# Kernel optimization log

Measured on AMD Instinct MI355X. Metric: run time of the kernel, lower is better.

Reference implementation:

```python
import jax, jax.numpy as jnp
import numpy as np

B, S, D, H = 2, 2048, 1024, 16
DK = D // H


def setup_inputs() -> dict:
    key = jax.random.key(0)
    ks = jax.random.split(key, 10)
    scale = 1.0 / np.sqrt(D)
    x = jax.random.normal(ks[0], (B, S, D), dtype=jnp.float32)
    # causal mask: 1 = attend, 0 = masked (module's create_causal_mask)
    mask = jnp.tril(jnp.ones((S, S), dtype=jnp.int32))[None, None]
    Wq = jax.random.normal(ks[1], (D, D), jnp.float32) * scale
    bq = jax.random.normal(ks[2], (D,), jnp.float32) * 0.01
    Wk = jax.random.normal(ks[3], (D, D), jnp.float32) * scale
    bk = jax.random.normal(ks[4], (D,), jnp.float32) * 0.01
    Wv = jax.random.normal(ks[5], (D, D), jnp.float32) * scale
    bv = jax.random.normal(ks[6], (D,), jnp.float32) * 0.01
    Wo = jax.random.normal(ks[7], (D, D), jnp.float32) * scale
    bo = jax.random.normal(ks[8], (D,), jnp.float32) * 0.01
    return {"x": x, "mask": mask, "Wq": Wq, "bq": bq, "Wk": Wk, "bk": bk,
            "Wv": Wv, "bv": bv, "Wo": Wo, "bo": bo}


def reference(x, mask, Wq, bq, Wk, bk, Wv, bv, Wo, bo):
    b, s, _ = x.shape
    # projections; [B,S,D] -> [B,H,S,DK]
    def split_heads(t):
        return t.reshape(b, s, H, DK).transpose(0, 2, 1, 3)
    Q = split_heads(x @ Wq + bq)
    K = split_heads(x @ Wk + bk)
    V = split_heads(x @ Wv + bv)
    scores = jnp.einsum('bhqd,bhkd->bhqk', Q, K) / np.sqrt(DK)
    scores = jnp.where(mask == 0, jnp.float32(-1e9), scores)
    attn = jax.nn.softmax(scores, axis=-1)  # dropout p=0 -> identity
    ctx = jnp.einsum('bhqk,bhkd->bhqd', attn, V)
    ctx = ctx.transpose(0, 2, 1, 3).reshape(b, s, D)
    return ctx @ Wo + bo
```

## Files before the change

### kernel.cpp

```cpp
#include <hip/hip_runtime.h>
#include <hip/hip_bf16.h>


typedef _Float16 f16x8 __attribute__((ext_vector_type(8)));
typedef _Float16 f16x4 __attribute__((ext_vector_type(4)));
typedef _Float16 f16x2 __attribute__((ext_vector_type(2)));
typedef float f32x4 __attribute__((ext_vector_type(4)));

#define QSCALE 0.180336880111112f

__device__ __forceinline__ void async_copy16(const _Float16* gsrc,
                                             _Float16* ldst) {
  __builtin_amdgcn_global_load_lds(
      (const __attribute__((address_space(1))) void*)gsrc,
      (__attribute__((address_space(3))) void*)ldst, 16, 0, 0);
}

__global__ __launch_bounds__(256) void prep(
    const float* __restrict__ x, _Float16* __restrict__ xh,
    const float* __restrict__ W0, const float* __restrict__ W1,
    const float* __restrict__ W2, const float* __restrict__ W3,
    _Float16* __restrict__ T0, _Float16* __restrict__ T1,
    _Float16* __restrict__ T2, _Float16* __restrict__ T3) {
  if (blockIdx.x < 4096) {
    int i = (blockIdx.x * 256 + threadIdx.x) * 4;
    float4 v = *(const float4*)(x + i);
    f16x4 o;
    o.x = (_Float16)v.x; o.y = (_Float16)v.y;
    o.z = (_Float16)v.z; o.w = (_Float16)v.w;
    *(f16x4*)(xh + i) = o;
    return;
  }
  const int id = blockIdx.x - 4096;
  const int w = id >> 10, rem = id & 1023;
  const int bx = rem & 31, by = rem >> 5;
  const float* W; _Float16* T;
  switch (w) {
    case 0: W = W0; T = T0; break;
    case 1: W = W1; T = T1; break;
    case 2: W = W2; T = T2; break;
    default: W = W3; T = T3; break;
  }
  __shared__ _Float16 tile[32][33];
  const int tx = threadIdx.x & 31, ty = threadIdx.x >> 5;
  const int n0 = bx * 32, k0 = by * 32;
  for (int i = 0; i < 4; i++) {
    int kk = k0 + ty + i * 8;
    tile[ty + i * 8][tx] = (_Float16)W[(size_t)kk * 1024 + n0 + tx];
  }
  __syncthreads();
  for (int i = 0; i < 4; i++) {
    int nn = n0 + ty + i * 8;
    T[(size_t)nn * 1024 + k0 + tx] = tile[tx][ty + i * 8];
  }
}

__global__ __launch_bounds__(256) void gemm_qkv(
    const _Float16* __restrict__ A, const _Float16* __restrict__ BtAll,
    const float* __restrict__ bq, const float* __restrict__ bk,
    const float* __restrict__ bv, _Float16* __restrict__ Qh,
    _Float16* __restrict__ Kh, _Float16* __restrict__ VT) {
  __shared__ _Float16 As[128 * 32];
  __shared__ _Float16 Bs[128 * 32];
  __shared__ _Float16 tbuf[64 * 136];
  const int tid = threadIdx.x;
  const int wave = tid >> 6, lane = tid & 63;
  const int lr = lane & 15, lq = lane >> 4;
  const int m0 = blockIdx.x * 128, n0 = blockIdx.y * 128;
  const int rw = (wave & 1) * 64, cw = (wave >> 1) * 64;

  const int sel = blockIdx.y >> 3;
  const float* bias = sel == 0 ? bq : (sel == 1 ? bk : bv);
  const int c0 = n0 & 1023;

  f32x4 acc[4][4] = {};
  const int r0 = wave * 32 + (lane >> 2);
  const int woff = (lane & 3) * 8;

  for (int kt = 0; kt < 1024; kt += 32) {
    __syncthreads();
    async_copy16(A + (size_t)(m0 + r0) * 1024 + kt + woff, As + r0 * 32 + woff);
    async_copy16(A + (size_t)(m0 + r0 + 16) * 1024 + kt + woff,
                 As + (r0 + 16) * 32 + woff);
    async_copy16(BtAll + (size_t)(n0 + r0) * 1024 + kt + woff,
                 Bs + r0 * 32 + woff);
    async_copy16(BtAll + (size_t)(n0 + r0 + 16) * 1024 + kt + woff,
                 Bs + (r0 + 16) * 32 + woff);
    __syncthreads();
    f16x8 af[4], bf[4];
    for (int i = 0; i < 4; i++)
      af[i] = *(const f16x8*)(As + (rw + i * 16 + lr) * 32 + lq * 8);
    for (int j = 0; j < 4; j++)
      bf[j] = *(const f16x8*)(Bs + (cw + j * 16 + lr) * 32 + lq * 8);
    for (int i = 0; i < 4; i++)
      for (int j = 0; j < 4; j++)
        acc[i][j] = __builtin_amdgcn_mfma_f32_16x16x32_f16(af[i], bf[j],
                                                           acc[i][j], 0, 0, 0);
  }

  if (sel == 2) {
    const int bb = m0 >> 11, ss0 = m0 & 2047;
    const int cs = tid & 15, dkr = tid >> 4;
    for (int jj = 0; jj < 2; jj++) {
      __syncthreads();
      if ((wave >> 1) == jj) {
        for (int i = 0; i < 4; i++) {
          const int sl = rw + i * 16 + lq * 4;
          for (int j = 0; j < 4; j++) {
            const int dk = j * 16 + lr;
            const float bvl = bias[c0 + jj * 64 + dk];
            f16x4 pv;
            for (int r = 0; r < 4; r++) pv[r] = (_Float16)(acc[i][j][r] + bvl);
            *(f16x4*)(tbuf + dk * 136 + sl) = pv;
          }
        }
      }
      __syncthreads();
      const int hh = (c0 + jj * 64) >> 6;
      _Float16* dst = VT + ((size_t)(bb * 16 + hh) * 64) * 2048 + ss0;
      for (int k = 0; k < 4; k++) {
        const int dk = dkr + k * 16;
        *(uint4*)(dst + (size_t)dk * 2048 + cs * 8) =
            *(const uint4*)(tbuf + dk * 136 + cs * 8);
      }
    }
  } else {
    _Float16* out = sel == 0 ? Qh : Kh;
    const float scl = sel == 0 ? QSCALE : 1.0f;
    for (int i = 0; i < 4; i++) {
      const int row = m0 + rw + i * 16 + lq * 4;
      for (int j = 0; j < 4; j++) {
        const int col = c0 + cw + j * 16 + lr;
        const float bvl = bias[col];
        for (int r = 0; r < 4; r++)
          out[(size_t)(row + r) * 1024 + col] =
              (_Float16)((acc[i][j][r] + bvl) * scl);
      }
    }
  }
}

__global__ __launch_bounds__(256) void gemm_out(
    const _Float16* __restrict__ A, const _Float16* __restrict__ Bt,
    const float* __restrict__ bias, float* __restrict__ out) {
  __shared__ _Float16 As[128 * 32];
  __shared__ _Float16 Bs[64 * 32];
  const int tid = threadIdx.x;
  const int wave = tid >> 6, lane = tid & 63;
  const int lr = lane & 15, lq = lane >> 4;
  const int m0 = blockIdx.x * 128, n0 = blockIdx.y * 64;
  const int rw = (wave & 1) * 64, cw = (wave >> 1) * 32;
  f32x4 acc[4][2] = {};
  const int r0 = wave * 32 + (lane >> 2);
  const int br = tid >> 2;
  const int woff = (lane & 3) * 8;

  for (int kt = 0; kt < 1024; kt += 32) {
    __syncthreads();
    async_copy16(A + (size_t)(m0 + r0) * 1024 + kt + woff, As + r0 * 32 + woff);
    async_copy16(A + (size_t)(m0 + r0 + 16) * 1024 + kt + woff,
                 As + (r0 + 16) * 32 + woff);
    async_copy16(Bt + (size_t)(n0 + br) * 1024 + kt + woff,
                 Bs + br * 32 + woff);
    __syncthreads();
    f16x8 af[4], bf[2];
    for (int i = 0; i < 4; i++)
      af[i] = *(const f16x8*)(As + (rw + i * 16 + lr) * 32 + lq * 8);
    for (int j = 0; j < 2; j++)
      bf[j] = *(const f16x8*)(Bs + (cw + j * 16 + lr) * 32 + lq * 8);
    for (int i = 0; i < 4; i++)
      for (int j = 0; j < 2; j++)
        acc[i][j] = __builtin_amdgcn_mfma_f32_16x16x32_f16(af[i], bf[j],
                                                           acc[i][j], 0, 0, 0);
  }
  for (int i = 0; i < 4; i++) {
    const int row = m0 + rw + i * 16 + lq * 4;
    for (int j = 0; j < 2; j++) {
      const int col = n0 + cw + j * 16 + lr;
      const float bvl = bias[col];
      for (int r = 0; r < 4; r++)
        out[(size_t)(row + r) * 1024 + col] = acc[i][j][r] + bvl;
    }
  }
}

__global__ __launch_bounds__(512, 4) void attn(const _Float16* __restrict__ Q,
                                               const _Float16* __restrict__ K,
                                               const _Float16* __restrict__ VT,
                                               _Float16* __restrict__ ctx) {
  const int sp = blockIdx.y;
  const int bh = blockIdx.x;
  const int b = bh >> 4, h = bh & 15;
  const int tid = threadIdx.x, wave = tid >> 6, lane = tid & 63;
  const int lr = lane & 15, lq = lane >> 4;
  const int rg = wave & 1;
  const int kvq = wave >> 1;
  const int kho = kvq * 16;
  const size_t qkbase = ((size_t)b * 2048) * 1024 + h * 64;
  const size_t vtbase = ((size_t)bh) * 64 * 2048;

  __shared__ __align__(16) char smem[45056];

  f16x4 onesf;
  {
    _Float16 ov = (lr == 0) ? (_Float16)1.0f : (_Float16)0.0f;
    for (int i = 0; i < 4; i++) onesf[i] = ov;
  }

  const int sgr = tid >> 3, sc8 = tid & 7;
  const int ssw = sgr * 64 + ((sc8 ^ (sgr & 7)) * 8);
  const _Float16* Kg0 = K + qkbase + (size_t)sgr * 1024 + sc8 * 8;
  const _Float16* Vg0 = VT + vtbase + (size_t)sgr * 2048 + sc8 * 8;

  for (int ph = 0; ph < 2; ph++) {
    const int st = ph ? 31 - sp : sp;
    const int qmin = st * 64 + rg * 32;
    const _Float16* qp = Q + qkbase + (size_t)(qmin + lr) * 1024 + lq * 8;
    f16x8 qA0 = *(const f16x8*)qp;
    f16x8 qA1 = *(const f16x8*)(qp + 32);
    f16x8 qB0 = *(const f16x8*)(qp + (size_t)16 * 1024);
    f16x8 qB1 = *(const f16x8*)(qp + (size_t)16 * 1024 + 32);

    f32x4 oA[4] = {}, oB[4] = {};
    f32x4 olA = {}, olB = {};

    uint4 ka = *(const uint4*)Kg0;
    uint4 va = *(const uint4*)Vg0;

    for (int t = 0; t <= st; t++) {
      _Float16* ksb = (_Float16*)(smem + (t & 1) * 8192);
      _Float16* vsb = (_Float16*)(smem + 16384 + (t & 1) * 8192);
      *(uint4*)(ksb + ssw) = ka;
      *(uint4*)(vsb + ssw) = va;
      __syncthreads();
      if (t < st) {
        const _Float16* kg = Kg0 + (size_t)(t + 1) * 64 * 1024;
        const _Float16* vg = Vg0 + (t + 1) * 64;
        ka = *(const uint4*)kg;
        va = *(const uint4*)vg;
      }
      const int kvw = t * 64 + kho;
      if (kvw > qmin + 31) continue;

      const int krow = kho + lr;
      const int ksw = krow & 7;
      f16x8 k0 = *(const f16x8*)(ksb + krow * 64 + ((lq ^ ksw) * 8));
      f16x8 k1 = *(const f16x8*)(ksb + krow * 64 + (((lq + 4) ^ ksw) * 8));

      f32x4 sA = {}, sB = {};
      sA = __builtin_amdgcn_mfma_f32_16x16x32_f16(k0, qA0, sA, 0, 0, 0);
      sA = __builtin_amdgcn_mfma_f32_16x16x32_f16(k1, qA1, sA, 0, 0, 0);
      sB = __builtin_amdgcn_mfma_f32_16x16x32_f16(k0, qB0, sB, 0, 0, 0);
      sB = __builtin_amdgcn_mfma_f32_16x16x32_f16(k1, qB1, sB, 0, 0, 0);

      if (kvw + 15 > qmin) {
        const int qcol = qmin + lr;
        for (int r = 0; r < 4; r++)
          if (kvw + lq * 4 + r > qcol) sA[r] = -1e30f;
      }
      if (kvw + 15 > qmin + 16) {
        const int qcol = qmin + 16 + lr;
        for (int r = 0; r < 4; r++)
          if (kvw + lq * 4 + r > qcol) sB[r] = -1e30f;
      }

      f16x4 paA, paB;
      {
        float p0 = exp2f(sA[0]), p1 = exp2f(sA[1]);
        float p2 = exp2f(sA[2]), p3 = exp2f(sA[3]);
        f16x2 q01 =
            __builtin_bit_cast(f16x2, __builtin_amdgcn_cvt_pkrtz(p0, p1));
        f16x2 q23 =
            __builtin_bit_cast(f16x2, __builtin_amdgcn_cvt_pkrtz(p2, p3));
        paA = __builtin_shufflevector(q01, q23, 0, 1, 2, 3);
      }
      {
        float p0 = exp2f(sB[0]), p1 = exp2f(sB[1]);
        float p2 = exp2f(sB[2]), p3 = exp2f(sB[3]);
        f16x2 q01 =
            __builtin_bit_cast(f16x2, __builtin_amdgcn_cvt_pkrtz(p0, p1));
        f16x2 q23 =
            __builtin_bit_cast(f16x2, __builtin_amdgcn_cvt_pkrtz(p2, p3));
        paB = __builtin_shufflevector(q01, q23, 0, 1, 2, 3);
      }

      __builtin_amdgcn_s_setprio(1);
      const int vc8 = kvq * 2 + (lq >> 1), vsub = (lq & 1) * 4;
      for (int dn = 0; dn < 4; dn++) {
        const int vrow = dn * 16 + lr;
        f16x4 vf = *(const f16x4*)(vsb + vrow * 64 +
                                   ((vc8 ^ (vrow & 7)) * 8) + vsub);
        oA[dn] = __builtin_amdgcn_mfma_f32_16x16x16f16(paA, vf, oA[dn], 0, 0, 0);
        oB[dn] = __builtin_amdgcn_mfma_f32_16x16x16f16(paB, vf, oB[dn], 0, 0, 0);
      }
      olA = __builtin_amdgcn_mfma_f32_16x16x16f16(paA, onesf, olA, 0, 0, 0);
      olB = __builtin_amdgcn_mfma_f32_16x16x16f16(paB, onesf, olB, 0, 0, 0);
      __builtin_amdgcn_s_setprio(0);
    }

    float* const cb = (float*)smem;
    __syncthreads();
    if (kvq == 1 || kvq == 3) {
      float* p = cb + (((kvq == 1 ? 0 : 2) + rg) * 64 + lane) * 44;
      *(f32x4*)(p + 0) = oA[0];  *(f32x4*)(p + 4) = oA[1];
      *(f32x4*)(p + 8) = oA[2];  *(f32x4*)(p + 12) = oA[3];
      *(f32x4*)(p + 16) = oB[0]; *(f32x4*)(p + 20) = oB[1];
      *(f32x4*)(p + 24) = oB[2]; *(f32x4*)(p + 28) = oB[3];
      *(f32x4*)(p + 32) = olA;   *(f32x4*)(p + 36) = olB;
    }
    __syncthreads();
    if (kvq == 0 || kvq == 2) {
      float* p = cb + (((kvq == 0 ? 0 : 2) + rg) * 64 + lane) * 44;
      oA[0] += *(const f32x4*)(p + 0);  oA[1] += *(const f32x4*)(p + 4);
      oA[2] += *(const f32x4*)(p + 8);  oA[3] += *(const f32x4*)(p + 12);
      oB[0] += *(const f32x4*)(p + 16); oB[1] += *(const f32x4*)(p + 20);
      oB[2] += *(const f32x4*)(p + 24); oB[3] += *(const f32x4*)(p + 28);
      olA += *(const f32x4*)(p + 32);   olB += *(const f32x4*)(p + 36);
      if (kvq == 2) {
        *(f32x4*)(p + 0) = oA[0];  *(f32x4*)(p + 4) = oA[1];
        *(f32x4*)(p + 8) = oA[2];  *(f32x4*)(p + 12) = oA[3];
        *(f32x4*)(p + 16) = oB[0]; *(f32x4*)(p + 20) = oB[1];
        *(f32x4*)(p + 24) = oB[2]; *(f32x4*)(p + 28) = oB[3];
        *(f32x4*)(p + 32) = olA;   *(f32x4*)(p + 36) = olB;
      }
    }
    __syncthreads();
    if (kvq == 0) {
      const float* p = cb + ((2 + rg) * 64 + lane) * 44;
      oA[0] += *(const f32x4*)(p + 0);  oA[1] += *(const f32x4*)(p + 4);
      oA[2] += *(const f32x4*)(p + 8);  oA[3] += *(const f32x4*)(p + 12);
      oB[0] += *(const f32x4*)(p + 16); oB[1] += *(const f32x4*)(p + 20);
      oB[2] += *(const f32x4*)(p + 24); oB[3] += *(const f32x4*)(p + 28);
      olA += *(const f32x4*)(p + 32);   olB += *(const f32x4*)(p + 36);
      for (int r = 0; r < 4; r++) {
        float lvA = __shfl(olA[r], lane & 48);
        float invA = 1.0f / lvA;
        const int rowA = qmin + lq * 4 + r;
        for (int dn = 0; dn < 4; dn++)
          ctx[qkbase + (size_t)rowA * 1024 + dn * 16 + lr] =
              (_Float16)(oA[dn][r] * invA);
        float lvB = __shfl(olB[r], lane & 48);
        float invB = 1.0f / lvB;
        const int rowB = qmin + 16 + lq * 4 + r;
        for (int dn = 0; dn < 4; dn++)
          ctx[qkbase + (size_t)rowB * 1024 + dn * 16 + lr] =
              (_Float16)(oB[dn][r] * invB);
      }
    }
    __syncthreads();
  }
}

extern "C" void kernel_launch(void* const* d_in, const int* in_sizes, int n_in,
                              void* d_out, int out_size, void* d_ws,
                              size_t ws_size, hipStream_t stream) {
  const float* x  = (const float*)d_in[0];
  const float* Wq = (const float*)d_in[2];
  const float* bq = (const float*)d_in[3];
  const float* Wk = (const float*)d_in[4];
  const float* bk = (const float*)d_in[5];
  const float* Wv = (const float*)d_in[6];
  const float* bv = (const float*)d_in[7];
  const float* Wo = (const float*)d_in[8];
  const float* bo = (const float*)d_in[9];
  float* out = (float*)d_out;

  char* ws = (char*)d_ws;
  const size_t MB = 1 << 20;
  _Float16* xh  = (_Float16*)(ws);
  _Float16* WTs = (_Float16*)(ws + 8 * MB);
  _Float16* WqT = WTs;
  _Float16* WkT = (_Float16*)(ws + 10 * MB);
  _Float16* WvT = (_Float16*)(ws + 12 * MB);
  _Float16* WoT = (_Float16*)(ws + 14 * MB);
  _Float16* Qh  = (_Float16*)(ws + 16 * MB);
  _Float16* Kh  = (_Float16*)(ws + 24 * MB);
  _Float16* VT  = (_Float16*)(ws + 32 * MB);
  _Float16* ctx = (_Float16*)(ws);

  prep<<<8192, 256, 0, stream>>>(x, xh, Wq, Wk, Wv, Wo, WqT, WkT, WvT, WoT);
  gemm_qkv<<<dim3(32, 24), 256, 0, stream>>>(xh, WTs, bq, bk, bv, Qh, Kh, VT);
  attn<<<dim3(32, 16), 512, 0, stream>>>(Qh, Kh, VT, ctx);
  gemm_out<<<dim3(32, 16), 256, 0, stream>>>(ctx, WoT, bo, out);
}
```

Measured before the change: 191.0 us.

## Enlarge attention KV tile to 128 keys per barrier step

Each loop iteration now stages 128 keys of K and V^T into double-buffered shared memory instead of 64, and each wave handles two 16-key slices inside an unrolled inner loop. This halves the number of __syncthreads barriers and global-to-LDS staging rounds per query tile, which cuts synchronisation overhead. In exchange shared memory rises from 44 KB to 64 KB per block, which may reduce occupancy under the 4-blocks launch bound, and the causal edge wastes more work on partially masked tiles.

```diff
diff --git a/kernel.cpp b/kernel.cpp
--- a/kernel.cpp
+++ b/kernel.cpp
@@ -195,11 +195,10 @@
   const int lr = lane & 15, lq = lane >> 4;
   const int rg = wave & 1;
   const int kvq = wave >> 1;
-  const int kho = kvq * 16;
   const size_t qkbase = ((size_t)b * 2048) * 1024 + h * 64;
   const size_t vtbase = ((size_t)bh) * 64 * 2048;
 
-  __shared__ __align__(16) char smem[45056];
+  __shared__ __align__(16) char smem[65536];
 
   f16x4 onesf;
   {
@@ -207,10 +206,14 @@
     for (int i = 0; i < 4; i++) onesf[i] = ov;
   }
 
-  const int sgr = tid >> 3, sc8 = tid & 7;
-  const int ssw = sgr * 64 + ((sc8 ^ (sgr & 7)) * 8);
-  const _Float16* Kg0 = K + qkbase + (size_t)sgr * 1024 + sc8 * 8;
-  const _Float16* Vg0 = VT + vtbase + (size_t)sgr * 2048 + sc8 * 8;
+  const int kr = tid >> 2, kc = tid & 3;
+  const int kw0 = kr * 64 + ((kc ^ (kr & 7)) * 8);
+  const int kw1 = kr * 64 + (((kc + 4) ^ (kr & 7)) * 8);
+  const _Float16* Kg0 = K + qkbase + (size_t)kr * 1024 + kc * 8;
+  const int vr = tid >> 3, vc = tid & 7;
+  const int vw0 = vr * 128 + ((vc ^ (vr & 7)) * 8);
+  const int vw1 = vr * 128 + (((vc + 8) ^ (vr & 7)) * 8);
+  const _Float16* Vg0 = VT + vtbase + (size_t)vr * 2048 + vc * 8;
 
   for (int ph = 0; ph < 2; ph++) {
     const int st = ph ? 31 - sp : sp;
@@ -224,78 +227,89 @@
     f32x4 oA[4] = {}, oB[4] = {};
     f32x4 olA = {}, olB = {};
 
-    uint4 ka = *(const uint4*)Kg0;
-    uint4 va = *(const uint4*)Vg0;
-
-    for (int t = 0; t <= st; t++) {
-      _Float16* ksb = (_Float16*)(smem + (t & 1) * 8192);
-      _Float16* vsb = (_Float16*)(smem + 16384 + (t & 1) * 8192);
-      *(uint4*)(ksb + ssw) = ka;
-      *(uint4*)(vsb + ssw) = va;
+    const int tmax = (st * 64 + 63) >> 7;
+
+    uint4 ka0 = *(const uint4*)Kg0, ka1 = *(const uint4*)(Kg0 + 32);
+    uint4 va0 = *(const uint4*)Vg0, va1 = *(const uint4*)(Vg0 + 64);
+
+    for (int t = 0; t <= tmax; t++) {
+      _Float16* ksb = (_Float16*)(smem + (t & 1) * 16384);
+      _Float16* vsb = (_Float16*)(smem + 32768 + (t & 1) * 16384);
+      *(uint4*)(ksb + kw0) = ka0;
+      *(uint4*)(ksb + kw1) = ka1;
+      *(uint4*)(vsb + vw0) = va0;
+      *(uint4*)(vsb + vw1) = va1;
       __syncthreads();
-      if (t < st) {
-        const _Float16* kg = Kg0 + (size_t)(t + 1) * 64 * 1024;
-        const _Float16* vg = Vg0 + (t + 1) * 64;
-        ka = *(const uint4*)kg;
-        va = *(const uint4*)vg;
-      }
-      const int kvw = t * 64 + kho;
-      if (kvw > qmin + 31) continue;
-
-      const int krow = kho + lr;
-      const int ksw = krow & 7;
-      f16x8 k0 = *(const f16x8*)(ksb + krow * 64 + ((lq ^ ksw) * 8));
-      f16x8 k1 = *(const f16x8*)(ksb + krow * 64 + (((lq + 4) ^ ksw) * 8));
-
-      f32x4 sA = {}, sB = {};
-      sA = __builtin_amdgcn_mfma_f32_16x16x32_f16(k0, qA0, sA, 0, 0, 0);
-      sA = __builtin_amdgcn_mfma_f32_16x16x32_f16(k1, qA1, sA, 0, 0, 0);
-      sB = __builtin_amdgcn_mfma_f32_16x16x32_f16(k0, qB0, sB, 0, 0, 0);
-      sB = __builtin_amdgcn_mfma_f32_16x16x32_f16(k1, qB1, sB, 0, 0, 0);
-
-      if (kvw + 15 > qmin) {
-        const int qcol = qmin + lr;
-        for (int r = 0; r < 4; r++)
-          if (kvw + lq * 4 + r > qcol) sA[r] = -1e30f;
-      }
-      if (kvw + 15 > qmin + 16) {
-        const int qcol = qmin + 16 + lr;
-        for (int r = 0; r < 4; r++)
-          if (kvw + lq * 4 + r > qcol) sB[r] = -1e30f;
-      }
-
-      f16x4 paA, paB;
-      {
-        float p0 = exp2f(sA[0]), p1 = exp2f(sA[1]);
-        float p2 = exp2f(sA[2]), p3 = exp2f(sA[3]);
-        f16x2 q01 =
-            __builtin_bit_cast(f16x2, __builtin_amdgcn_cvt_pkrtz(p0, p1));
-        f16x2 q23 =
-            __builtin_bit_cast(f16x2, __builtin_amdgcn_cvt_pkrtz(p2, p3));
-        paA = __builtin_shufflevector(q01, q23, 0, 1, 2, 3);
-      }
-      {
-        float p0 = exp2f(sB[0]), p1 = exp2f(sB[1]);
-        float p2 = exp2f(sB[2]), p3 = exp2f(sB[3]);
-        f16x2 q01 =
-            __builtin_bit_cast(f16x2, __builtin_amdgcn_cvt_pkrtz(p0, p1));
-        f16x2 q23 =
-            __builtin_bit_cast(f16x2, __builtin_amdgcn_cvt_pkrtz(p2, p3));
-        paB = __builtin_shufflevector(q01, q23, 0, 1, 2, 3);
-      }
-
-      __builtin_amdgcn_s_setprio(1);
-      const int vc8 = kvq * 2 + (lq >> 1), vsub = (lq & 1) * 4;
-      for (int dn = 0; dn < 4; dn++) {
-        const int vrow = dn * 16 + lr;
-        f16x4 vf = *(const f16x4*)(vsb + vrow * 64 +
-                                   ((vc8 ^ (vrow & 7)) * 8) + vsub);
-        oA[dn] = __builtin_amdgcn_mfma_f32_16x16x16f16(paA, vf, oA[dn], 0, 0, 0);
-        oB[dn] = __builtin_amdgcn_mfma_f32_16x16x16f16(paB, vf, oB[dn], 0, 0, 0);
-      }
-      olA = __builtin_amdgcn_mfma_f32_16x16x16f16(paA, onesf, olA, 0, 0, 0);
-      olB = __builtin_amdgcn_mfma_f32_16x16x16f16(paB, onesf, olB, 0, 0, 0);
-      __builtin_amdgcn_s_setprio(0);
+      if (t < tmax) {
+        const _Float16* kg = Kg0 + (size_t)(t + 1) * 131072;
+        const _Float16* vg = Vg0 + (t + 1) * 128;
+        ka0 = *(const uint4*)kg; ka1 = *(const uint4*)(kg + 32);
+        va0 = *(const uint4*)vg; va1 = *(const uint4*)(vg + 64);
+      }
+      if (t * 128 + kvq * 32 > qmin + 31) continue;
+
+#pragma unroll
+      for (int ksl = 0; ksl < 2; ksl++) {
+        const int kvw = t * 128 + kvq * 32 + ksl * 16;
+        if (kvw > qmin + 31) break;
+
+        const int krow = kvq * 32 + ksl * 16 + lr;
+        const int ksw = krow & 7;
+        f16x8 k0 = *(const f16x8*)(ksb + krow * 64 + ((lq ^ ksw) * 8));
+        f16x8 k1 = *(const f16x8*)(ksb + krow * 64 + (((lq + 4) ^ ksw) * 8));
+
+        f32x4 sA = {}, sB = {};
+        sA = __builtin_amdgcn_mfma_f32_16x16x32_f16(k0, qA0, sA, 0, 0, 0);
+        sA = __builtin_amdgcn_mfma_f32_16x16x32_f16(k1, qA1, sA, 0, 0, 0);
+        sB = __builtin_amdgcn_mfma_f32_16x16x32_f16(k0, qB0, sB, 0, 0, 0);
+        sB = __builtin_amdgcn_mfma_f32_16x16x32_f16(k1, qB1, sB, 0, 0, 0);
+
+        if (kvw + 15 > qmin) {
+          const int qcol = qmin + lr;
+          for (int r = 0; r < 4; r++)
+            if (kvw + lq * 4 + r > qcol) sA[r] = -1e30f;
+        }
+        if (kvw + 15 > qmin + 16) {
+          const int qcol = qmin + 16 + lr;
+          for (int r = 0; r < 4; r++)
+            if (kvw + lq * 4 + r > qcol) sB[r] = -1e30f;
+        }
+
+        f16x4 paA, paB;
+        {
+          float p0 = exp2f(sA[0]), p1 = exp2f(sA[1]);
+          float p2 = exp2f(sA[2]), p3 = exp2f(sA[3]);
+          f16x2 q01 =
+              __builtin_bit_cast(f16x2, __builtin_amdgcn_cvt_pkrtz(p0, p1));
+          f16x2 q23 =
+              __builtin_bit_cast(f16x2, __builtin_amdgcn_cvt_pkrtz(p2, p3));
+          paA = __builtin_shufflevector(q01, q23, 0, 1, 2, 3);
+        }
+        {
+          float p0 = exp2f(sB[0]), p1 = exp2f(sB[1]);
+          float p2 = exp2f(sB[2]), p3 = exp2f(sB[3]);
+          f16x2 q01 =
+              __builtin_bit_cast(f16x2, __builtin_amdgcn_cvt_pkrtz(p0, p1));
+          f16x2 q23 =
+              __builtin_bit_cast(f16x2, __builtin_amdgcn_cvt_pkrtz(p2, p3));
+          paB = __builtin_shufflevector(q01, q23, 0, 1, 2, 3);
+        }
+
+        __builtin_amdgcn_s_setprio(1);
+        const int vc8 = kvq * 4 + ksl * 2 + (lq >> 1), vsub = (lq & 1) * 4;
+        for (int dn = 0; dn < 4; dn++) {
+          const int vrow = dn * 16 + lr;
+          f16x4 vf = *(const f16x4*)(vsb + vrow * 128 +
+                                     ((vc8 ^ (vrow & 7)) * 8) + vsub);
+          oA[dn] =
+              __builtin_amdgcn_mfma_f32_16x16x16f16(paA, vf, oA[dn], 0, 0, 0);
+          oB[dn] =
+              __builtin_amdgcn_mfma_f32_16x16x16f16(paB, vf, oB[dn], 0, 0, 0);
+        }
+        olA = __builtin_amdgcn_mfma_f32_16x16x16f16(paA, onesf, olA, 0, 0, 0);
+        olB = __builtin_amdgcn_mfma_f32_16x16x16f16(paB, onesf, olB, 0, 0, 0);
+        __builtin_amdgcn_s_setprio(0);
+      }
     }
 
     float* const cb = (float*)smem;
```

New measurement: 196.1 us. +2.7%, slower.

## Split attention blocks into 32-row query tiles with 4 waves per block

Applied to the files above, without the earlier changes.

The attention kernel now uses 256-thread blocks that each handle one 32-row query tile, instead of 512-thread blocks covering two 32-row groups of a 64-row tile. The grid doubles to 32x32, and causal pairing now runs over 64 tiles (j and 63-j). Each thread stages two 16-byte chunks of K and V per step, and shared memory drops to 32 KB. The aim is finer-grained load balance and higher occupancy. The cost is that K/V tiles are reloaded from global memory twice as often across blocks.

```diff
diff --git a/kernel.cpp b/kernel.cpp
--- a/kernel.cpp
+++ b/kernel.cpp
@@ -184,7 +184,7 @@
   }
 }
 
-__global__ __launch_bounds__(512, 4) void attn(const _Float16* __restrict__ Q,
+__global__ __launch_bounds__(256, 4) void attn(const _Float16* __restrict__ Q,
                                                const _Float16* __restrict__ K,
                                                const _Float16* __restrict__ VT,
                                                _Float16* __restrict__ ctx) {
@@ -193,13 +193,12 @@
   const int b = bh >> 4, h = bh & 15;
   const int tid = threadIdx.x, wave = tid >> 6, lane = tid & 63;
   const int lr = lane & 15, lq = lane >> 4;
-  const int rg = wave & 1;
-  const int kvq = wave >> 1;
+  const int kvq = wave;
   const int kho = kvq * 16;
   const size_t qkbase = ((size_t)b * 2048) * 1024 + h * 64;
   const size_t vtbase = ((size_t)bh) * 64 * 2048;
 
-  __shared__ __align__(16) char smem[45056];
+  __shared__ __align__(16) char smem[32768];
 
   f16x4 onesf;
   {
@@ -207,14 +206,15 @@
     for (int i = 0; i < 4; i++) onesf[i] = ov;
   }
 
-  const int sgr = tid >> 3, sc8 = tid & 7;
-  const int ssw = sgr * 64 + ((sc8 ^ (sgr & 7)) * 8);
-  const _Float16* Kg0 = K + qkbase + (size_t)sgr * 1024 + sc8 * 8;
-  const _Float16* Vg0 = VT + vtbase + (size_t)sgr * 2048 + sc8 * 8;
+  const int sgr = tid >> 2, sc = tid & 3;
+  const int sw0 = sgr * 64 + ((sc ^ (sgr & 7)) * 8);
+  const int sw1 = sgr * 64 + (((sc + 4) ^ (sgr & 7)) * 8);
+  const _Float16* Kg0 = K + qkbase + (size_t)sgr * 1024 + sc * 8;
+  const _Float16* Vg0 = VT + vtbase + (size_t)sgr * 2048 + sc * 8;
 
   for (int ph = 0; ph < 2; ph++) {
-    const int st = ph ? 31 - sp : sp;
-    const int qmin = st * 64 + rg * 32;
+    const int j = ph ? 63 - sp : sp;
+    const int qmin = j * 32;
     const _Float16* qp = Q + qkbase + (size_t)(qmin + lr) * 1024 + lq * 8;
     f16x8 qA0 = *(const f16x8*)qp;
     f16x8 qA1 = *(const f16x8*)(qp + 32);
@@ -224,20 +224,24 @@
     f32x4 oA[4] = {}, oB[4] = {};
     f32x4 olA = {}, olB = {};
 
-    uint4 ka = *(const uint4*)Kg0;
-    uint4 va = *(const uint4*)Vg0;
-
-    for (int t = 0; t <= st; t++) {
+    const int tmax = (qmin + 31) >> 6;
+
+    uint4 ka = *(const uint4*)Kg0, kb = *(const uint4*)(Kg0 + 32);
+    uint4 va = *(const uint4*)Vg0, vb = *(const uint4*)(Vg0 + 32);
+
+    for (int t = 0; t <= tmax; t++) {
       _Float16* ksb = (_Float16*)(smem + (t & 1) * 8192);
       _Float16* vsb = (_Float16*)(smem + 16384 + (t & 1) * 8192);
-      *(uint4*)(ksb + ssw) = ka;
-      *(uint4*)(vsb + ssw) = va;
+      *(uint4*)(ksb + sw0) = ka;
+      *(uint4*)(ksb + sw1) = kb;
+      *(uint4*)(vsb + sw0) = va;
+      *(uint4*)(vsb + sw1) = vb;
       __syncthreads();
-      if (t < st) {
-        const _Float16* kg = Kg0 + (size_t)(t + 1) * 64 * 1024;
+      if (t < tmax) {
+        const _Float16* kg = Kg0 + (size_t)(t + 1) * 65536;
         const _Float16* vg = Vg0 + (t + 1) * 64;
-        ka = *(const uint4*)kg;
-        va = *(const uint4*)vg;
+        ka = *(const uint4*)kg; kb = *(const uint4*)(kg + 32);
+        va = *(const uint4*)vg; vb = *(const uint4*)(vg + 32);
       }
       const int kvw = t * 64 + kho;
       if (kvw > qmin + 31) continue;
@@ -300,8 +304,8 @@
 
     float* const cb = (float*)smem;
     __syncthreads();
-    if (kvq == 1 || kvq == 3) {
-      float* p = cb + (((kvq == 1 ? 0 : 2) + rg) * 64 + lane) * 44;
+    if (wave & 1) {
+      float* p = cb + ((wave >> 1) * 64 + lane) * 44;
       *(f32x4*)(p + 0) = oA[0];  *(f32x4*)(p + 4) = oA[1];
       *(f32x4*)(p + 8) = oA[2];  *(f32x4*)(p + 12) = oA[3];
       *(f32x4*)(p + 16) = oB[0]; *(f32x4*)(p + 20) = oB[1];
@@ -309,14 +313,14 @@
       *(f32x4*)(p + 32) = olA;   *(f32x4*)(p + 36) = olB;
     }
     __syncthreads();
-    if (kvq == 0 || kvq == 2) {
-      float* p = cb + (((kvq == 0 ? 0 : 2) + rg) * 64 + lane) * 44;
+    if (!(wave & 1)) {
+      float* p = cb + ((wave >> 1) * 64 + lane) * 44;
       oA[0] += *(const f32x4*)(p + 0);  oA[1] += *(const f32x4*)(p + 4);
       oA[2] += *(const f32x4*)(p + 8);  oA[3] += *(const f32x4*)(p + 12);
       oB[0] += *(const f32x4*)(p + 16); oB[1] += *(const f32x4*)(p + 20);
       oB[2] += *(const f32x4*)(p + 24); oB[3] += *(const f32x4*)(p + 28);
       olA += *(const f32x4*)(p + 32);   olB += *(const f32x4*)(p + 36);
-      if (kvq == 2) {
+      if (wave == 2) {
         *(f32x4*)(p + 0) = oA[0];  *(f32x4*)(p + 4) = oA[1];
         *(f32x4*)(p + 8) = oA[2];  *(f32x4*)(p + 12) = oA[3];
         *(f32x4*)(p + 16) = oB[0]; *(f32x4*)(p + 20) = oB[1];
@@ -325,8 +329,8 @@
       }
     }
     __syncthreads();
-    if (kvq == 0) {
-      const float* p = cb + ((2 + rg) * 64 + lane) * 44;
+    if (wave == 0) {
+      const float* p = cb + (64 + lane) * 44;
       oA[0] += *(const f32x4*)(p + 0);  oA[1] += *(const f32x4*)(p + 4);
       oA[2] += *(const f32x4*)(p + 8);  oA[3] += *(const f32x4*)(p + 12);
       oB[0] += *(const f32x4*)(p + 16); oB[1] += *(const f32x4*)(p + 20);
@@ -380,6 +384,6 @@
 
   prep<<<8192, 256, 0, stream>>>(x, xh, Wq, Wk, Wv, Wo, WqT, WkT, WvT, WoT);
   gemm_qkv<<<dim3(32, 24), 256, 0, stream>>>(xh, WTs, bq, bk, bv, Qh, Kh, VT);
-  attn<<<dim3(32, 16), 512, 0, stream>>>(Qh, Kh, VT, ctx);
+  attn<<<dim3(32, 32), 256, 0, stream>>>(Qh, Kh, VT, ctx);
   gemm_out<<<dim3(32, 16), 256, 0, stream>>>(ctx, WoT, bo, out);
 }
```

New measurement: 197.6 us. 3.5% more time.

## Double GEMM K-tile to 64 with XOR-swizzled LDS layout

Applied to the files above, without the earlier changes.

Both the QKV and output-projection GEMMs now stage 64-wide K tiles instead of 32, halving the number of barrier pairs per K loop. Global columns are XOR-swizzled by row on load so the fragment reads from LDS avoid bank conflicts with the wider 128-byte rows. The QKV kernel also aliases its transpose buffer onto the same shared memory, keeping LDS use at 32KB. The trade-off is a larger LDS footprint per block, which may reduce occupancy, and the loop is still single-buffered with no prefetch.

```diff
diff --git a/kernel.cpp b/kernel.cpp
--- a/kernel.cpp
+++ b/kernel.cpp
@@ -60,9 +60,9 @@
     const float* __restrict__ bq, const float* __restrict__ bk,
     const float* __restrict__ bv, _Float16* __restrict__ Qh,
     _Float16* __restrict__ Kh, _Float16* __restrict__ VT) {
-  __shared__ _Float16 As[128 * 32];
-  __shared__ _Float16 Bs[128 * 32];
-  __shared__ _Float16 tbuf[64 * 136];
+  __shared__ __align__(16) char smem[32768];
+  _Float16* As = (_Float16*)smem;
+  _Float16* Bs = (_Float16*)(smem + 16384);
   const int tid = threadIdx.x;
   const int wave = tid >> 6, lane = tid & 63;
   const int lr = lane & 15, lq = lane >> 4;
@@ -74,31 +74,42 @@
   const int c0 = n0 & 1023;
 
   f32x4 acc[4][4] = {};
-  const int r0 = wave * 32 + (lane >> 2);
-  const int woff = (lane & 3) * 8;
-
-  for (int kt = 0; kt < 1024; kt += 32) {
-    __syncthreads();
-    async_copy16(A + (size_t)(m0 + r0) * 1024 + kt + woff, As + r0 * 32 + woff);
-    async_copy16(A + (size_t)(m0 + r0 + 16) * 1024 + kt + woff,
-                 As + (r0 + 16) * 32 + woff);
-    async_copy16(BtAll + (size_t)(n0 + r0) * 1024 + kt + woff,
-                 Bs + r0 * 32 + woff);
-    async_copy16(BtAll + (size_t)(n0 + r0 + 16) * 1024 + kt + woff,
-                 Bs + (r0 + 16) * 32 + woff);
-    __syncthreads();
-    f16x8 af[4], bf[4];
-    for (int i = 0; i < 4; i++)
-      af[i] = *(const f16x8*)(As + (rw + i * 16 + lr) * 32 + lq * 8);
-    for (int j = 0; j < 4; j++)
-      bf[j] = *(const f16x8*)(Bs + (cw + j * 16 + lr) * 32 + lq * 8);
-    for (int i = 0; i < 4; i++)
-      for (int j = 0; j < 4; j++)
-        acc[i][j] = __builtin_amdgcn_mfma_f32_16x16x32_f16(af[i], bf[j],
-                                                           acc[i][j], 0, 0, 0);
+  const int sr = lane >> 3;
+  const int srow = wave * 32 + sr;
+  const int sgc = (((lane & 7) ^ sr)) * 8;
+  const int sldst = srow * 64 + (lane & 7) * 8;
+  const int lrx = lr & 7;
+
+  for (int kt = 0; kt < 1024; kt += 64) {
+    __syncthreads();
+#pragma unroll
+    for (int off = 0; off < 32; off += 8) {
+      async_copy16(A + (size_t)(m0 + srow + off) * 1024 + kt + sgc,
+                   As + sldst + off * 64);
+      async_copy16(BtAll + (size_t)(n0 + srow + off) * 1024 + kt + sgc,
+                   Bs + sldst + off * 64);
+    }
+    __syncthreads();
+#pragma unroll
+    for (int kk = 0; kk < 2; kk++) {
+      f16x8 af[4], bf[4];
+      for (int i = 0; i < 4; i++) {
+        const int ar = rw + i * 16 + lr;
+        af[i] = *(const f16x8*)(As + ar * 64 + (((kk * 4 + lq) ^ lrx) * 8));
+      }
+      for (int j = 0; j < 4; j++) {
+        const int br = cw + j * 16 + lr;
+        bf[j] = *(const f16x8*)(Bs + br * 64 + (((kk * 4 + lq) ^ lrx) * 8));
+      }
+      for (int i = 0; i < 4; i++)
+        for (int j = 0; j < 4; j++)
+          acc[i][j] = __builtin_amdgcn_mfma_f32_16x16x32_f16(
+              af[i], bf[j], acc[i][j], 0, 0, 0);
+    }
   }
 
   if (sel == 2) {
+    _Float16* tbuf = (_Float16*)smem;
     const int bb = m0 >> 11, ss0 = m0 & 2047;
     const int cs = tid & 15, dkr = tid >> 4;
     for (int jj = 0; jj < 2; jj++) {
@@ -143,35 +154,50 @@
 __global__ __launch_bounds__(256) void gemm_out(
     const _Float16* __restrict__ A, const _Float16* __restrict__ Bt,
     const float* __restrict__ bias, float* __restrict__ out) {
-  __shared__ _Float16 As[128 * 32];
-  __shared__ _Float16 Bs[64 * 32];
+  __shared__ __align__(16) char smem[24576];
+  _Float16* As = (_Float16*)smem;
+  _Float16* Bs = (_Float16*)(smem + 16384);
   const int tid = threadIdx.x;
   const int wave = tid >> 6, lane = tid & 63;
   const int lr = lane & 15, lq = lane >> 4;
   const int m0 = blockIdx.x * 128, n0 = blockIdx.y * 64;
   const int rw = (wave & 1) * 64, cw = (wave >> 1) * 32;
   f32x4 acc[4][2] = {};
-  const int r0 = wave * 32 + (lane >> 2);
-  const int br = tid >> 2;
-  const int woff = (lane & 3) * 8;
-
-  for (int kt = 0; kt < 1024; kt += 32) {
-    __syncthreads();
-    async_copy16(A + (size_t)(m0 + r0) * 1024 + kt + woff, As + r0 * 32 + woff);
-    async_copy16(A + (size_t)(m0 + r0 + 16) * 1024 + kt + woff,
-                 As + (r0 + 16) * 32 + woff);
-    async_copy16(Bt + (size_t)(n0 + br) * 1024 + kt + woff,
-                 Bs + br * 32 + woff);
-    __syncthreads();
-    f16x8 af[4], bf[2];
-    for (int i = 0; i < 4; i++)
-      af[i] = *(const f16x8*)(As + (rw + i * 16 + lr) * 32 + lq * 8);
-    for (int j = 0; j < 2; j++)
-      bf[j] = *(const f16x8*)(Bs + (cw + j * 16 + lr) * 32 + lq * 8);
-    for (int i = 0; i < 4; i++)
-      for (int j = 0; j < 2; j++)
-        acc[i][j] = __builtin_amdgcn_mfma_f32_16x16x32_f16(af[i], bf[j],
-                                                           acc[i][j], 0, 0, 0);
+  const int sr = lane >> 3;
+  const int srow = wave * 32 + sr;
+  const int brow = wave * 8 + sr;
+  const int sgc = (((lane & 7) ^ sr)) * 8;
+  const int sldstA = srow * 64 + (lane & 7) * 8;
+  const int sldstB = brow * 64 + (lane & 7) * 8;
+  const int lrx = lr & 7;
+
+  for (int kt = 0; kt < 1024; kt += 64) {
+    __syncthreads();
+#pragma unroll
+    for (int off = 0; off < 32; off += 8) {
+      async_copy16(A + (size_t)(m0 + srow + off) * 1024 + kt + sgc,
+                   As + sldstA + off * 64);
+    }
+    async_copy16(Bt + (size_t)(n0 + brow) * 1024 + kt + sgc, Bs + sldstB);
+    async_copy16(Bt + (size_t)(n0 + brow + 32) * 1024 + kt + sgc,
+                 Bs + sldstB + 32 * 64);
+    __syncthreads();
+#pragma unroll
+    for (int kk = 0; kk < 2; kk++) {
+      f16x8 af[4], bf[2];
+      for (int i = 0; i < 4; i++) {
+        const int ar = rw + i * 16 + lr;
+        af[i] = *(const f16x8*)(As + ar * 64 + (((kk * 4 + lq) ^ lrx) * 8));
+      }
+      for (int j = 0; j < 2; j++) {
+        const int br = cw + j * 16 + lr;
+        bf[j] = *(const f16x8*)(Bs + br * 64 + (((kk * 4 + lq) ^ lrx) * 8));
+      }
+      for (int i = 0; i < 4; i++)
+        for (int j = 0; j < 2; j++)
+          acc[i][j] = __builtin_amdgcn_mfma_f32_16x16x32_f16(
+              af[i], bf[j], acc[i][j], 0, 0, 0);
+    }
   }
   for (int i = 0; i < 4; i++) {
     const int row = m0 + rw + i * 16 + lq * 4;
```

Result: slower. 196.4 us (+2.9%).
